# Kernel optimization log

Measured on AMD Instinct MI355X. Metric: run time of the kernel, lower is better.

## Reference

```python
import jax, jax.numpy as jnp
import numpy as np

TOP_K = 48
NUM_RBF = 16
MAX_REL = 32  # max_relative_feature


def _rbf(D):
    # D: [...], expand into NUM_RBF Gaussian basis functions over [2, 22] Angstrom
    mu = jnp.linspace(2.0, 22.0, NUM_RBF)
    sigma = (22.0 - 2.0) / NUM_RBF
    return jnp.exp(-(((D[..., None] - mu) / sigma) ** 2))


def _gather_nodes(C, E_idx):
    # C: [B,L,3], E_idx: [B,L,K] -> [B,L,K,3]
    return jax.vmap(lambda c, idx: c[idx])(C, E_idx)


def _pair_rbf(A, Bc, E_idx):
    # RBF of ||A_i - Bc_j|| for j in neighbors(i); identical math to torch's
    # full [B,L,L] cdist followed by gather_edges, but gathers coords first.
    Bg = _gather_nodes(Bc, E_idx)
    D = jnp.sqrt(jnp.sum((A[:, :, None, :] - Bg) ** 2, -1) + 1e-6)
    return _rbf(D)


def setup_inputs() -> dict:
    key = jax.random.key(0)
    ks = jax.random.split(key, 8)
    B, L = 4, 1024
    X = jax.random.normal(ks[0], (B, L, 4, 3), jnp.float32)
    mask = jnp.ones((B, L), jnp.float32)
    residue_idx = jnp.arange(B * L, dtype=jnp.int32).reshape(B, L)
    chain_labels = jax.random.randint(ks[1], (B, L), 0, 4, dtype=jnp.int32)
    W_pos = jax.random.normal(ks[2], (16, 2 * MAX_REL + 2), jnp.float32) * 0.1
    b_pos = jnp.zeros((16,), jnp.float32)
    W_edge = jax.random.normal(ks[3], (128, 16 + 25 * NUM_RBF), jnp.float32) * 0.05
    ln_g = jnp.ones((128,), jnp.float32)
    ln_b = jnp.zeros((128,), jnp.float32)
    return dict(X=X, mask=mask, residue_idx=residue_idx, chain_labels=chain_labels,
                W_pos=W_pos, b_pos=b_pos, W_edge=W_edge, ln_g=ln_g, ln_b=ln_b)


def reference(X, mask, residue_idx, chain_labels, W_pos, b_pos, W_edge, ln_g, ln_b):
    # backbone atoms
    N = X[:, :, 0]; Ca = X[:, :, 1]; C = X[:, :, 2]; O = X[:, :, 3]
    b = Ca - N
    c = C - Ca
    a = jnp.cross(b, c)
    Cb = -0.58273431 * a + 0.56802827 * b - 0.54067466 * c + Ca

    # _dist: masked Ca-Ca pairwise distances, k nearest neighbors
    mask2 = mask[:, None, :] * mask[:, :, None]          # [B,L,L]
    dX = Ca[:, None, :, :] - Ca[:, :, None, :]
    D = mask2 * jnp.sqrt(jnp.sum(dX ** 2, -1) + 1e-6)
    D_max = jnp.max(D, -1, keepdims=True)
    D_adjust = D + (1.0 - mask2) * D_max
    K = min(TOP_K, X.shape[1])
    negD, E_idx = jax.lax.top_k(-D_adjust, K)            # smallest-K distances
    D_neighbors = -negD                                  # [B,L,K]

    # 25 atom-pair RBF blocks (order matches torch source)
    pairs = [(N, N), (C, C), (O, O), (Cb, Cb), (Ca, N), (Ca, C), (Ca, O), (Ca, Cb),
             (N, C), (N, O), (N, Cb), (Cb, C), (Cb, O), (O, C), (N, Ca), (C, Ca),
             (O, Ca), (Cb, Ca), (C, N), (O, N), (Cb, N), (C, Cb), (O, Cb), (C, O)]
    RBFs = [_rbf(D_neighbors)] + [_pair_rbf(A, Bc, E_idx) for A, Bc in pairs]
    RBFs = jnp.concatenate(RBFs, -1)                     # [B,L,K,25*NUM_RBF]

    # positional encodings
    offset = residue_idx[:, :, None] - residue_idx[:, None, :]
    offset = jnp.take_along_axis(offset, E_idx, axis=2)  # [B,L,K]
    d_chains = (chain_labels[:, :, None] == chain_labels[:, None, :]).astype(jnp.int32)
    E_chains = jnp.take_along_axis(d_chains, E_idx, axis=2)
    d = jnp.clip(offset + MAX_REL, 0, 2 * MAX_REL)
    d = d * E_chains + (1 - E_chains) * (2 * MAX_REL + 1)
    # one_hot(d, 66) @ W_pos.T + b_pos == row gather of W_pos.T
    E_pos = W_pos.T[d] + b_pos                           # [B,L,K,16]

    E = jnp.concatenate([E_pos, RBFs], -1)               # [B,L,K,416]
    E = jnp.einsum('blkf,ef->blke', E, W_edge)           # edge_embedding (no bias)
    mu = jnp.mean(E, -1, keepdims=True)
    var = jnp.var(E, -1, keepdims=True)
    E = (E - mu) / jnp.sqrt(var + 1e-5) * ln_g + ln_b    # LayerNorm
    return E, E_idx
```

## Files before the change

kernel.cpp:

```cpp
#include <hip/hip_runtime.h>
#include <stdint.h>

#define LSEQ 1024
#define NB 4
#define KNB 48
#define NFEAT 416
#define NOUT 128
#define NNODE (NB*LSEQ)

typedef float f32x4 __attribute__((ext_vector_type(4)));
typedef short s16x8 __attribute__((ext_vector_type(8)));

__device__ float4 g_atoms[NNODE*5];
__device__ ushort g_wbf[NOUT*NFEAT];
__device__ ushort g_wpt[66*16];
__device__ int    g_nbr[NNODE*KNB];
__device__ float  g_dnb[NNODE*KNB];

__constant__ int cPA[24] = {0,2,3,4,1,1,1,1,0,0,0,4,4,3,0,2,3,4,2,3,4,2,3,2};
__constant__ int cPB[24] = {0,2,3,4,0,2,3,4,2,3,4,2,3,2,1,1,1,1,0,0,0,4,4,3};

__device__ __forceinline__ ushort f2bf(float x) {
  unsigned u = __float_as_uint(x);
  u += 0x7fffu + ((u >> 16) & 1u);
  return (ushort)(u >> 16);
}
__device__ __forceinline__ unsigned pack2bf(float lo, float hi) {
  return __builtin_amdgcn_perm(__float_as_uint(hi), __float_as_uint(lo), 0x07060302u);
}

#define DPP_ADD_F(x, CTRL) { int _y = __builtin_amdgcn_mov_dpp(__float_as_int(x), CTRL, 0xF, 0xF, true); x += __int_as_float(_y); }
#define DPP_MIN_U(x, CTRL) { unsigned _y = (unsigned)__builtin_amdgcn_mov_dpp((int)(x), CTRL, 0xF, 0xF, true); x = min(x, _y); }

__device__ __forceinline__ unsigned wave_umin(unsigned x) {
  DPP_MIN_U(x, 0x128) DPP_MIN_U(x, 0x124) DPP_MIN_U(x, 0x122) DPP_MIN_U(x, 0x121)
  x = min(x, (unsigned)__shfl_xor((int)x, 16, 64));
  x = min(x, (unsigned)__shfl_xor((int)x, 32, 64));
  return x;
}

__global__ __launch_bounds__(256) void k_front(
    const float* __restrict__ X, const float* __restrict__ mask,
    const float* __restrict__ W, const float* __restrict__ Wpos,
    const float* __restrict__ bpos, float* __restrict__ outIdx)
{
  __shared__ float4 sca[LSEQ];
  __shared__ unsigned qhi[4][64][17];
  __shared__ unsigned qlo[4][64][17];
  int blk = blockIdx.x, tid = threadIdx.x;

  if (blk >= 1024) {
    int pb = blk - 1024;
    if (pb < 16) {
      int t = pb*256 + tid;
      const float* p = X + (size_t)t*12;
      float nx=p[0],ny=p[1],nz=p[2];
      float cax=p[3],cay=p[4],caz=p[5];
      float cx=p[6],cy=p[7],cz=p[8];
      float ox=p[9],oy=p[10],oz=p[11];
      float bx=cax-nx, by=cay-ny, bz=caz-nz;
      float ex=cx-cax, ey=cy-cay, ez=cz-caz;
      float ax2 = by*ez - bz*ey;
      float ay2 = bz*ex - bx*ez;
      float az2 = bx*ey - by*ex;
      float cbx = -0.58273431f*ax2 + 0.56802827f*bx - 0.54067466f*ex + cax;
      float cby = -0.58273431f*ay2 + 0.56802827f*by - 0.54067466f*ey + cay;
      float cbz = -0.58273431f*az2 + 0.56802827f*bz - 0.54067466f*ez + caz;
      g_atoms[t*5+0] = make_float4(nx,ny,nz,0.f);
      g_atoms[t*5+1] = make_float4(cax,cay,caz,0.f);
      g_atoms[t*5+2] = make_float4(cx,cy,cz,0.f);
      g_atoms[t*5+3] = make_float4(ox,oy,oz,0.f);
      g_atoms[t*5+4] = make_float4(cbx,cby,cbz,0.f);
    } else if (pb < 32) {
      int base = (pb-16)*3328 + tid;
      #pragma unroll
      for (int q = 0; q < 13; ++q) g_wbf[base + q*256] = f2bf(W[base + q*256]);
    } else {
      for (int t = tid; t < 66*16; t += 256) {
        int d = t >> 4, c = t & 15;
        g_wpt[t] = f2bf(Wpos[c*66 + d] + bpos[c]);
      }
    }
    return;
  }

  int b = blk >> 8, chunk = blk & 255;
  for (int t = tid; t < LSEQ; t += 256) {
    const float* p = X + (size_t)(b*LSEQ + t)*12 + 3;
    sca[t] = make_float4(p[0], p[1], p[2], mask[b*LSEQ + t]);
  }
  __syncthreads();
  int wv = tid >> 6, lane = tid & 63;
  int i = chunk*4 + wv;
  float4 ci = sca[i];
  float  mi = ci.w;

  float Dv[16]; float dmax = 0.f;
  #pragma unroll
  for (int q = 0; q < 16; ++q) {
    int j = lane + (q << 6);
    float4 cj = sca[j];
    float dx = __fsub_rn(cj.x, ci.x);
    float dy = __fsub_rn(cj.y, ci.y);
    float dz = __fsub_rn(cj.z, ci.z);
    float s  = __fadd_rn(__fadd_rn(__fmul_rn(dx,dx), __fmul_rn(dy,dy)), __fmul_rn(dz,dz));
    float sq = __fsqrt_rn(__fadd_rn(s, 1e-6f));
    float d  = __fmul_rn(__fmul_rn(mi, cj.w), sq);
    Dv[q] = d;
    dmax = fmaxf(dmax, d);
  }
  #pragma unroll
  for (int o = 32; o; o >>= 1) dmax = fmaxf(dmax, __shfl_xor(dmax, o, 64));

  unsigned long long key[16];
  #pragma unroll
  for (int q = 0; q < 16; ++q) {
    int j = lane + (q << 6);
    float m2   = __fmul_rn(mi, sca[j].w);
    float dadj = __fadd_rn(Dv[q], __fmul_rn(__fsub_rn(1.0f, m2), dmax));
    key[q] = ((unsigned long long)__float_as_uint(dadj) << 32) | (unsigned)j;
  }

  #pragma unroll
  for (int p = 1; p < 16; p <<= 1)
    #pragma unroll
    for (int k = p; k >= 1; k >>= 1)
      #pragma unroll
      for (int j = k & (p - 1); j + k < 16; j += 2*k)
        #pragma unroll
        for (int u = 0; u < k; ++u)
          if (u + j + k < 16 && ((u + j) / (2*p) == (u + j + k) / (2*p))) {
            unsigned long long a = key[u+j], c2 = key[u+j+k];
            if (a > c2) { key[u+j] = c2; key[u+j+k] = a; }
          }

  #pragma unroll
  for (int q = 0; q < 16; ++q) {
    qhi[wv][lane][q] = (unsigned)(key[q] >> 32);
    qlo[wv][lane][q] = (unsigned)key[q];
  }

  unsigned hhi = (unsigned)(key[0] >> 32), hlo = (unsigned)key[0];
  int pos = 0;
  size_t row = (size_t)(b*LSEQ + i);
  for (int k = 0; k < KNB; ++k) {
    unsigned mh = wave_umin(hhi);
    unsigned long long bmask = __ballot(hhi == mh);
    bool own;
    if (__popcll(bmask) == 1) {
      own = (hhi == mh);
    } else {
      unsigned jv = (hhi == mh) ? hlo : 0xFFFFFFFFu;
      unsigned mj = wave_umin(jv);
      own = (hhi == mh) && (hlo == mj);
    }
    if (own) {
      g_nbr[row*KNB + k] = (int)hlo;
      g_dnb[row*KNB + k] = __uint_as_float(mh);
      outIdx[row*KNB + k] = (float)(int)hlo;
      ++pos;
      if (pos < 16) { hhi = qhi[wv][lane][pos]; hlo = qlo[wv][lane][pos]; }
      else          { hhi = 0xFFFFFFFFu; hlo = 0xFFFFFFFFu; }
    }
  }
}

__global__ __launch_bounds__(256, 4) void k_edge(
    const int* __restrict__ ridx, const int* __restrict__ chain,
    const float* __restrict__ lng, const float* __restrict__ lnb,
    float* __restrict__ out)
{
  __shared__ __align__(16) ushort featb[KNB*256];
  __shared__ float4 atN[KNB*5];
  __shared__ float4 atI[5];
  __shared__ float  sdn[KNB];
  __shared__ int    sdd[KNB];
  __shared__ float2 sstat[KNB][4];
  __shared__ float2 rstat[KNB];

  int node = blockIdx.x;
  int b = node >> 10;
  size_t ebase = (size_t)node * KNB;
  int t = threadIdx.x;

  if (t < KNB) {
    int j = g_nbr[ebase + t];
    sdn[t] = g_dnb[ebase + t];
    int off = ridx[node] - ridx[b*LSEQ + j];
    bool same = (chain[node] == chain[b*LSEQ + j]);
    int dcl = min(max(off + 32, 0), 64);
    sdd[t] = same ? dcl : 65;
  }
  if (t >= 64 && t < 69) atI[t-64] = g_atoms[node*5 + (t-64)];
  for (int u = t; u < KNB*5; u += 256) {
    int k = u / 5, a = u % 5;
    atN[u] = g_atoms[(b*LSEQ + g_nbr[ebase + k])*5 + a];
  }
  __syncthreads();

  auto rbf_store = [&](int k, int slot, float d) {
    const float DLT  = 1.28119724f;
    const float TDLT = 2.56239448f;
    const float NDSQ = -1.64146638f;
    const float INVK = 0.10274013f;
    float u0  = __fmaf_rn(d, 0.96089793f, -1.92179585f);
    float u15 = u0 - 19.21795854f;
    float e[16];
    float eA = __builtin_amdgcn_exp2f(-(u0*u0));
    float rA = __builtin_amdgcn_exp2f(__fmaf_rn(u0, TDLT, NDSQ));
    float eB = __builtin_amdgcn_exp2f(-(u15*u15));
    float rB = __builtin_amdgcn_exp2f(__fmaf_rn(u15, -TDLT, NDSQ));
    e[0] = eA; e[15] = eB;
    #pragma unroll
    for (int j2 = 1; j2 < 8; ++j2) {
      eA *= rA; rA *= INVK; e[j2] = eA;
      eB *= rB; rB *= INVK; e[15-j2] = eB;
    }
    union { s16x8 v; unsigned w[4]; } a0, a1;
    #pragma unroll
    for (int q = 0; q < 4; ++q) {
      a0.w[q] = pack2bf(e[2*q],   e[2*q+1]);
      a1.w[q] = pack2bf(e[8+2*q], e[8+2*q+1]);
    }
    ushort* fp = &featb[k*256 + ((slot ^ (k & 7)) << 4)];
    *(s16x8*)fp       = a0.v;
    *(s16x8*)(fp + 8) = a1.v;
  };

  if (t < 96) {
    int k = t >> 1, h = t & 1;
    *(s16x8*)&featb[k*256 + ((0 ^ (k & 7)) << 4) + h*8] =
        *(const s16x8*)&g_wpt[sdd[k]*16 + h*8];
  }
  for (int u = t; u < KNB*13; u += 256) {
    int k = u / 13, p = u % 13;
    float d;
    if (p == 0) d = sdn[k];
    else {
      float4 A = atI[cPA[p-1]];
      float4 Bv = atN[k*5 + cPB[p-1]];
      float dx = A.x-Bv.x, dy = A.y-Bv.y, dz = A.z-Bv.z;
      d = sqrtf(dx*dx + dy*dy + dz*dz + 1e-6f);
    }
    rbf_store(k, p + 1, d);
  }
  __syncthreads();

  int ln = t & 63, wv = t >> 6;
  int fr = ln & 15, fq = ln >> 4;
  int n0 = wv * 32;
  f32x4 acc[3][2];
  #pragma unroll
  for (int mt = 0; mt < 3; ++mt) { acc[mt][0] = (f32x4)0.f; acc[mt][1] = (f32x4)0.f; }
  const ushort* w0 = &g_wbf[(n0 + fr)*NFEAT];
  const ushort* w1 = &g_wbf[(n0 + 16 + fr)*NFEAT];

#define GEMM_PASS(WOFF, NSTEPS)                                                     \
  {                                                                                 \
    s16x8 cw0 = *(const s16x8*)&w0[(WOFF) + fq*8];                                  \
    s16x8 cw1 = *(const s16x8*)&w1[(WOFF) + fq*8];                                  \
    _Pragma("unroll")                                                               \
    for (int s = 0; s < (NSTEPS); ++s) {                                            \
      int kk = s*32 + fq*8;                                                         \
      s16x8 nw0, nw1;                                                               \
      if (s + 1 < (NSTEPS)) {                                                       \
        nw0 = *(const s16x8*)&w0[(WOFF) + kk + 32];                                 \
        nw1 = *(const s16x8*)&w1[(WOFF) + kk + 32];                                 \
      }                                                                             \
      _Pragma("unroll")                                                             \
      for (int mt = 0; mt < 3; ++mt) {                                              \
        int row = mt*16 + fr;                                                       \
        s16x8 af = *(const s16x8*)&featb[row*256 + (((kk >> 4) ^ (fr & 7)) << 4) + (kk & 8)]; \
        acc[mt][0] = __builtin_amdgcn_mfma_f32_16x16x32_bf16(af, cw0, acc[mt][0], 0, 0, 0);   \
        acc[mt][1] = __builtin_amdgcn_mfma_f32_16x16x32_bf16(af, cw1, acc[mt][1], 0, 0, 0);   \
      }                                                                             \
      if (s + 1 < (NSTEPS)) { cw0 = nw0; cw1 = nw1; }                               \
    }                                                                               \
  }

  GEMM_PASS(0, 7)
  __syncthreads();

  for (int u = t; u < KNB*12; u += 256) {
    int k = u / 12, p = 13 + u % 12;
    float4 A = atI[cPA[p-1]];
    float4 Bv = atN[k*5 + cPB[p-1]];
    float dx = A.x-Bv.x, dy = A.y-Bv.y, dz = A.z-Bv.z;
    rbf_store(k, p - 13, sqrtf(dx*dx + dy*dy + dz*dz + 1e-6f));
  }
  __syncthreads();

  GEMM_PASS(224, 6)

  #pragma unroll
  for (int mt = 0; mt < 3; ++mt)
    #pragma unroll
    for (int i2 = 0; i2 < 4; ++i2) {
      float v0 = acc[mt][0][i2], v1 = acc[mt][1][i2];
      float s = v0 + v1, sq = v0*v0 + v1*v1;
      DPP_ADD_F(s, 0x128) DPP_ADD_F(s, 0x124) DPP_ADD_F(s, 0x122) DPP_ADD_F(s, 0x121)
      DPP_ADD_F(sq, 0x128) DPP_ADD_F(sq, 0x124) DPP_ADD_F(sq, 0x122) DPP_ADD_F(sq, 0x121)
      if (fr == 0) sstat[mt*16 + fq*4 + i2][wv] = make_float2(s, sq);
    }
  __syncthreads();
  if (t < KNB) {
    float s = 0.f, sq = 0.f;
    #pragma unroll
    for (int w = 0; w < 4; ++w) { float2 pp = sstat[t][w]; s += pp.x; sq += pp.y; }
    float mu  = s * (1.0f/128.0f);
    float var = sq * (1.0f/128.0f) - mu*mu;
    rstat[t] = make_float2(mu, rsqrtf(var + 1e-5f));
  }
  __syncthreads();
  float gn0 = lng[n0+fr], gn1 = lng[n0+16+fr];
  float bn0 = lnb[n0+fr], bn1 = lnb[n0+16+fr];
  #pragma unroll
  for (int mt = 0; mt < 3; ++mt)
    #pragma unroll
    for (int i2 = 0; i2 < 4; ++i2) {
      int row = mt*16 + fq*4 + i2;
      float2 mr = rstat[row];
      size_t ob = (ebase + row) * NOUT;
      out[ob + n0 + fr]      = (acc[mt][0][i2] - mr.x) * mr.y * gn0 + bn0;
      out[ob + n0 + 16 + fr] = (acc[mt][1][i2] - mr.x) * mr.y * gn1 + bn1;
    }
}

extern "C" void kernel_launch(void* const* d_in, const int* in_sizes, int n_in,
                              void* d_out, int out_size, void* d_ws, size_t ws_size,
                              hipStream_t stream) {
  const float* X     = (const float*)d_in[0];
  const float* mask  = (const float*)d_in[1];
  const int*   ridx  = (const int*)d_in[2];
  const int*   chain = (const int*)d_in[3];
  const float* Wpos  = (const float*)d_in[4];
  const float* bpos  = (const float*)d_in[5];
  const float* Wedge = (const float*)d_in[6];
  const float* lng   = (const float*)d_in[7];
  const float* lnb   = (const float*)d_in[8];
  float* out = (float*)d_out;
  float* outIdx = out + (size_t)NNODE*KNB*NOUT;

  k_front<<<dim3(1024 + 33), dim3(256), 0, stream>>>(X, mask, Wedge, Wpos, bpos, outIdx);
  k_edge<<<dim3(NNODE), dim3(256), 0, stream>>>(ridx, chain, lng, lnb, out);
}
```

Before: 81.52 us.

## Split front kernel and replace sorted-queue top-k with per-lane min selection

The fused front kernel is split into separate prep, weight-convert and top-k kernels. The top-k no longer bitonic-sorts each lane's 16 keys into shared-memory queues. Instead each lane keeps only its running minimum, and the wave does a full 64-bit butterfly min reduction each iteration. The owning lane then rescans its 16 registers to find its next minimum. This removes the sort and the LDS queue traffic, but adds two extra kernel launches and a costlier 6-step 64-bit shuffle reduction on each of the 48 iterations.

```diff
diff --git a/kernel.cpp b/kernel.cpp
--- a/kernel.cpp
+++ b/kernel.cpp
@@ -12,6 +12,7 @@
 typedef short s16x8 __attribute__((ext_vector_type(8)));
 
 __device__ float4 g_atoms[NNODE*5];
+__device__ float4 g_ca[NNODE];
 __device__ ushort g_wbf[NOUT*NFEAT];
 __device__ ushort g_wpt[66*16];
 __device__ int    g_nbr[NNODE*KNB];
@@ -30,72 +31,68 @@
 }
 
 #define DPP_ADD_F(x, CTRL) { int _y = __builtin_amdgcn_mov_dpp(__float_as_int(x), CTRL, 0xF, 0xF, true); x += __int_as_float(_y); }
-#define DPP_MIN_U(x, CTRL) { unsigned _y = (unsigned)__builtin_amdgcn_mov_dpp((int)(x), CTRL, 0xF, 0xF, true); x = min(x, _y); }
-
-__device__ __forceinline__ unsigned wave_umin(unsigned x) {
-  DPP_MIN_U(x, 0x128) DPP_MIN_U(x, 0x124) DPP_MIN_U(x, 0x122) DPP_MIN_U(x, 0x121)
-  x = min(x, (unsigned)__shfl_xor((int)x, 16, 64));
-  x = min(x, (unsigned)__shfl_xor((int)x, 32, 64));
-  return x;
-}
-
-__global__ __launch_bounds__(256) void k_front(
-    const float* __restrict__ X, const float* __restrict__ mask,
-    const float* __restrict__ W, const float* __restrict__ Wpos,
-    const float* __restrict__ bpos, float* __restrict__ outIdx)
-{
+
+__device__ __forceinline__ unsigned long long shfl_xor_u64(unsigned long long x, int m) {
+  unsigned hi = __shfl_xor((unsigned)(x >> 32), m, 64);
+  unsigned lo = __shfl_xor((unsigned)(x & 0xffffffffu), m, 64);
+  return ((unsigned long long)hi << 32) | lo;
+}
+
+__global__ void k_prep(const float* __restrict__ X) {
+  int t = blockIdx.x*256 + threadIdx.x;
+  if (t >= NNODE) return;
+  const float* p = X + (size_t)t*12;
+  float nx=p[0],ny=p[1],nz=p[2];
+  float cax=p[3],cay=p[4],caz=p[5];
+  float cx=p[6],cy=p[7],cz=p[8];
+  float ox=p[9],oy=p[10],oz=p[11];
+  float bx=cax-nx, by=cay-ny, bz=caz-nz;
+  float ex=cx-cax, ey=cy-cay, ez=cz-caz;
+  float ax2 = by*ez - bz*ey;
+  float ay2 = bz*ex - bx*ez;
+  float az2 = bx*ey - by*ex;
+  float cbx = -0.58273431f*ax2 + 0.56802827f*bx - 0.54067466f*ex + cax;
+  float cby = -0.58273431f*ay2 + 0.56802827f*by - 0.54067466f*ey + cay;
+  float cbz = -0.58273431f*az2 + 0.56802827f*bz - 0.54067466f*ez + caz;
+  g_atoms[t*5+0] = make_float4(nx,ny,nz,0.f);
+  g_atoms[t*5+1] = make_float4(cax,cay,caz,0.f);
+  g_atoms[t*5+2] = make_float4(cx,cy,cz,0.f);
+  g_atoms[t*5+3] = make_float4(ox,oy,oz,0.f);
+  g_atoms[t*5+4] = make_float4(cbx,cby,cbz,0.f);
+  g_ca[t] = make_float4(cax,cay,caz,0.f);
+}
+
+__global__ void k_wcvt(const float* __restrict__ W, const float* __restrict__ Wpos,
+                       const float* __restrict__ bpos) {
+  int blk = blockIdx.x, tid = threadIdx.x;
+  if (blk < 208) {
+    int t = blk*256 + tid;
+    g_wbf[t] = f2bf(W[t]);
+  } else {
+    for (int t = tid; t < 66*16; t += 256) {
+      int d = t >> 4, c = t & 15;
+      g_wpt[t] = f2bf(Wpos[c*66 + d] + bpos[c]);
+    }
+  }
+}
+
+__global__ __launch_bounds__(256) void k_topk(const float* __restrict__ mask,
+                                              float* __restrict__ outIdx) {
   __shared__ float4 sca[LSEQ];
-  __shared__ unsigned qhi[4][64][17];
-  __shared__ unsigned qlo[4][64][17];
-  int blk = blockIdx.x, tid = threadIdx.x;
-
-  if (blk >= 1024) {
-    int pb = blk - 1024;
-    if (pb < 16) {
-      int t = pb*256 + tid;
-      const float* p = X + (size_t)t*12;
-      float nx=p[0],ny=p[1],nz=p[2];
-      float cax=p[3],cay=p[4],caz=p[5];
-      float cx=p[6],cy=p[7],cz=p[8];
-      float ox=p[9],oy=p[10],oz=p[11];
-      float bx=cax-nx, by=cay-ny, bz=caz-nz;
-      float ex=cx-cax, ey=cy-cay, ez=cz-caz;
-      float ax2 = by*ez - bz*ey;
-      float ay2 = bz*ex - bx*ez;
-      float az2 = bx*ey - by*ex;
-      float cbx = -0.58273431f*ax2 + 0.56802827f*bx - 0.54067466f*ex + cax;
-      float cby = -0.58273431f*ay2 + 0.56802827f*by - 0.54067466f*ey + cay;
-      float cbz = -0.58273431f*az2 + 0.56802827f*bz - 0.54067466f*ez + caz;
-      g_atoms[t*5+0] = make_float4(nx,ny,nz,0.f);
-      g_atoms[t*5+1] = make_float4(cax,cay,caz,0.f);
-      g_atoms[t*5+2] = make_float4(cx,cy,cz,0.f);
-      g_atoms[t*5+3] = make_float4(ox,oy,oz,0.f);
-      g_atoms[t*5+4] = make_float4(cbx,cby,cbz,0.f);
-    } else if (pb < 32) {
-      int base = (pb-16)*3328 + tid;
-      #pragma unroll
-      for (int q = 0; q < 13; ++q) g_wbf[base + q*256] = f2bf(W[base + q*256]);
-    } else {
-      for (int t = tid; t < 66*16; t += 256) {
-        int d = t >> 4, c = t & 15;
-        g_wpt[t] = f2bf(Wpos[c*66 + d] + bpos[c]);
-      }
-    }
-    return;
-  }
-
-  int b = blk >> 8, chunk = blk & 255;
-  for (int t = tid; t < LSEQ; t += 256) {
-    const float* p = X + (size_t)(b*LSEQ + t)*12 + 3;
-    sca[t] = make_float4(p[0], p[1], p[2], mask[b*LSEQ + t]);
-  }
-  __syncthreads();
-  int wv = tid >> 6, lane = tid & 63;
-  int i = chunk*4 + wv;
+  __shared__ float  sm[LSEQ];
+  int b = blockIdx.y;
+  for (int t = threadIdx.x; t < LSEQ; t += 256) {
+    sca[t] = g_ca[b*LSEQ + t];
+    sm[t]  = mask[b*LSEQ + t];
+  }
+  __syncthreads();
+  int wave = threadIdx.x >> 6, lane = threadIdx.x & 63;
+  int i = blockIdx.x*4 + wave;
   float4 ci = sca[i];
-  float  mi = ci.w;
-
-  float Dv[16]; float dmax = 0.f;
+  float  mi = sm[i];
+
+  float Dv[16];
+  float dmax = 0.f;
   #pragma unroll
   for (int q = 0; q < 16; ++q) {
     int j = lane + (q << 6);
@@ -105,7 +102,7 @@
     float dz = __fsub_rn(cj.z, ci.z);
     float s  = __fadd_rn(__fadd_rn(__fmul_rn(dx,dx), __fmul_rn(dy,dy)), __fmul_rn(dz,dz));
     float sq = __fsqrt_rn(__fadd_rn(s, 1e-6f));
-    float d  = __fmul_rn(__fmul_rn(mi, cj.w), sq);
+    float d  = __fmul_rn(__fmul_rn(mi, sm[j]), sq);
     Dv[q] = d;
     dmax = fmaxf(dmax, d);
   }
@@ -113,54 +110,38 @@
   for (int o = 32; o; o >>= 1) dmax = fmaxf(dmax, __shfl_xor(dmax, o, 64));
 
   unsigned long long key[16];
+  unsigned long long lmin = ~0ull;
   #pragma unroll
   for (int q = 0; q < 16; ++q) {
     int j = lane + (q << 6);
-    float m2   = __fmul_rn(mi, sca[j].w);
+    float m2   = __fmul_rn(mi, sm[j]);
     float dadj = __fadd_rn(Dv[q], __fmul_rn(__fsub_rn(1.0f, m2), dmax));
     key[q] = ((unsigned long long)__float_as_uint(dadj) << 32) | (unsigned)j;
-  }
-
-  #pragma unroll
-  for (int p = 1; p < 16; p <<= 1)
-    #pragma unroll
-    for (int k = p; k >= 1; k >>= 1)
-      #pragma unroll
-      for (int j = k & (p - 1); j + k < 16; j += 2*k)
-        #pragma unroll
-        for (int u = 0; u < k; ++u)
-          if (u + j + k < 16 && ((u + j) / (2*p) == (u + j + k) / (2*p))) {
-            unsigned long long a = key[u+j], c2 = key[u+j+k];
-            if (a > c2) { key[u+j] = c2; key[u+j+k] = a; }
-          }
-
-  #pragma unroll
-  for (int q = 0; q < 16; ++q) {
-    qhi[wv][lane][q] = (unsigned)(key[q] >> 32);
-    qlo[wv][lane][q] = (unsigned)key[q];
-  }
-
-  unsigned hhi = (unsigned)(key[0] >> 32), hlo = (unsigned)key[0];
-  int pos = 0;
+    lmin = (key[q] < lmin) ? key[q] : lmin;
+  }
+
   size_t row = (size_t)(b*LSEQ + i);
   for (int k = 0; k < KNB; ++k) {
-    unsigned mh = wave_umin(hhi);
-    unsigned long long bmask = __ballot(hhi == mh);
-    bool own;
-    if (__popcll(bmask) == 1) {
-      own = (hhi == mh);
-    } else {
-      unsigned jv = (hhi == mh) ? hlo : 0xFFFFFFFFu;
-      unsigned mj = wave_umin(jv);
-      own = (hhi == mh) && (hlo == mj);
-    }
-    if (own) {
-      g_nbr[row*KNB + k] = (int)hlo;
-      g_dnb[row*KNB + k] = __uint_as_float(mh);
-      outIdx[row*KNB + k] = (float)(int)hlo;
-      ++pos;
-      if (pos < 16) { hhi = qhi[wv][lane][pos]; hlo = qlo[wv][lane][pos]; }
-      else          { hhi = 0xFFFFFFFFu; hlo = 0xFFFFFFFFu; }
+    unsigned long long m = lmin;
+    #pragma unroll
+    for (int o = 1; o < 64; o <<= 1) {
+      unsigned long long other = shfl_xor_u64(m, o);
+      m = (other < m) ? other : m;
+    }
+    if (lane == 0) {
+      unsigned j = (unsigned)(m & 0xffffffffu);
+      g_nbr[row*KNB + k] = (int)j;
+      g_dnb[row*KNB + k] = __uint_as_float((unsigned)(m >> 32));
+      outIdx[row*KNB + k] = (float)(int)j;
+    }
+    if (m == lmin) {
+      unsigned long long nm = ~0ull;
+      #pragma unroll
+      for (int q = 0; q < 16; ++q) {
+        if (key[q] == m) key[q] = ~0ull;
+        nm = (key[q] < nm) ? key[q] : nm;
+      }
+      lmin = nm;
     }
   }
 }
@@ -199,7 +180,6 @@
   __syncthreads();
 
   auto rbf_store = [&](int k, int slot, float d) {
-    const float DLT  = 1.28119724f;
     const float TDLT = 2.56239448f;
     const float NDSQ = -1.64146638f;
     const float INVK = 0.10274013f;
@@ -341,6 +321,8 @@
   float* out = (float*)d_out;
   float* outIdx = out + (size_t)NNODE*KNB*NOUT;
 
-  k_front<<<dim3(1024 + 33), dim3(256), 0, stream>>>(X, mask, Wedge, Wpos, bpos, outIdx);
+  k_prep<<<dim3(NNODE/256), dim3(256), 0, stream>>>(X);
+  k_wcvt<<<dim3(209), dim3(256), 0, stream>>>(Wedge, Wpos, bpos);
+  k_topk<<<dim3(LSEQ/4, NB), dim3(256), 0, stream>>>(mask, outIdx);
   k_edge<<<dim3(NNODE), dim3(256), 0, stream>>>(ridx, chain, lng, lnb, out);
 }
```

After: 118.2 us. 1.45x slower.

## Fuse kNN top-k selection into edge kernel, drop neighbor index round trip

Applied to the files above, without the earlier changes.

Moves the Ca distance computation, bitonic sort and wave-level top-k merge out of the front kernel and into each edge block, where one wave selects the node's 48 neighbors into shared memory, reusing the feature buffer. A small preprocessing kernel now only builds atoms, Ca coordinates and bf16 weights. This removes the global writes and reads of neighbor indices and distances, along with a large front grid. In exchange, each edge block does its top-k in a single wave while the other three wait, which adds serial latency per block and may lengthen the edge kernel.

```diff
diff --git a/kernel.cpp b/kernel.cpp
--- a/kernel.cpp
+++ b/kernel.cpp
@@ -12,10 +12,9 @@
 typedef short s16x8 __attribute__((ext_vector_type(8)));
 
 __device__ float4 g_atoms[NNODE*5];
+__device__ float4 g_ca[NNODE];
 __device__ ushort g_wbf[NOUT*NFEAT];
 __device__ ushort g_wpt[66*16];
-__device__ int    g_nbr[NNODE*KNB];
-__device__ float  g_dnb[NNODE*KNB];
 
 __constant__ int cPA[24] = {0,2,3,4,1,1,1,1,0,0,0,4,4,3,0,2,3,4,2,3,4,2,3,2};
 __constant__ int cPB[24] = {0,2,3,4,0,2,3,4,2,3,4,2,3,2,1,1,1,1,0,0,0,4,4,3};
@@ -39,167 +38,162 @@
   return x;
 }
 
-__global__ __launch_bounds__(256) void k_front(
-    const float* __restrict__ X, const float* __restrict__ mask,
-    const float* __restrict__ W, const float* __restrict__ Wpos,
-    const float* __restrict__ bpos, float* __restrict__ outIdx)
-{
-  __shared__ float4 sca[LSEQ];
-  __shared__ unsigned qhi[4][64][17];
-  __shared__ unsigned qlo[4][64][17];
+__global__ void k_pre(const float* __restrict__ X, const float* __restrict__ W,
+                      const float* __restrict__ Wpos, const float* __restrict__ bpos) {
   int blk = blockIdx.x, tid = threadIdx.x;
-
-  if (blk >= 1024) {
-    int pb = blk - 1024;
-    if (pb < 16) {
-      int t = pb*256 + tid;
-      const float* p = X + (size_t)t*12;
-      float nx=p[0],ny=p[1],nz=p[2];
-      float cax=p[3],cay=p[4],caz=p[5];
-      float cx=p[6],cy=p[7],cz=p[8];
-      float ox=p[9],oy=p[10],oz=p[11];
-      float bx=cax-nx, by=cay-ny, bz=caz-nz;
-      float ex=cx-cax, ey=cy-cay, ez=cz-caz;
-      float ax2 = by*ez - bz*ey;
-      float ay2 = bz*ex - bx*ez;
-      float az2 = bx*ey - by*ex;
-      float cbx = -0.58273431f*ax2 + 0.56802827f*bx - 0.54067466f*ex + cax;
-      float cby = -0.58273431f*ay2 + 0.56802827f*by - 0.54067466f*ey + cay;
-      float cbz = -0.58273431f*az2 + 0.56802827f*bz - 0.54067466f*ez + caz;
-      g_atoms[t*5+0] = make_float4(nx,ny,nz,0.f);
-      g_atoms[t*5+1] = make_float4(cax,cay,caz,0.f);
-      g_atoms[t*5+2] = make_float4(cx,cy,cz,0.f);
-      g_atoms[t*5+3] = make_float4(ox,oy,oz,0.f);
-      g_atoms[t*5+4] = make_float4(cbx,cby,cbz,0.f);
-    } else if (pb < 32) {
-      int base = (pb-16)*3328 + tid;
-      #pragma unroll
-      for (int q = 0; q < 13; ++q) g_wbf[base + q*256] = f2bf(W[base + q*256]);
-    } else {
-      for (int t = tid; t < 66*16; t += 256) {
-        int d = t >> 4, c = t & 15;
-        g_wpt[t] = f2bf(Wpos[c*66 + d] + bpos[c]);
-      }
-    }
-    return;
-  }
-
-  int b = blk >> 8, chunk = blk & 255;
-  for (int t = tid; t < LSEQ; t += 256) {
-    const float* p = X + (size_t)(b*LSEQ + t)*12 + 3;
-    sca[t] = make_float4(p[0], p[1], p[2], mask[b*LSEQ + t]);
-  }
-  __syncthreads();
-  int wv = tid >> 6, lane = tid & 63;
-  int i = chunk*4 + wv;
-  float4 ci = sca[i];
-  float  mi = ci.w;
-
-  float Dv[16]; float dmax = 0.f;
-  #pragma unroll
-  for (int q = 0; q < 16; ++q) {
-    int j = lane + (q << 6);
-    float4 cj = sca[j];
-    float dx = __fsub_rn(cj.x, ci.x);
-    float dy = __fsub_rn(cj.y, ci.y);
-    float dz = __fsub_rn(cj.z, ci.z);
-    float s  = __fadd_rn(__fadd_rn(__fmul_rn(dx,dx), __fmul_rn(dy,dy)), __fmul_rn(dz,dz));
-    float sq = __fsqrt_rn(__fadd_rn(s, 1e-6f));
-    float d  = __fmul_rn(__fmul_rn(mi, cj.w), sq);
-    Dv[q] = d;
-    dmax = fmaxf(dmax, d);
-  }
-  #pragma unroll
-  for (int o = 32; o; o >>= 1) dmax = fmaxf(dmax, __shfl_xor(dmax, o, 64));
-
-  unsigned long long key[16];
-  #pragma unroll
-  for (int q = 0; q < 16; ++q) {
-    int j = lane + (q << 6);
-    float m2   = __fmul_rn(mi, sca[j].w);
-    float dadj = __fadd_rn(Dv[q], __fmul_rn(__fsub_rn(1.0f, m2), dmax));
-    key[q] = ((unsigned long long)__float_as_uint(dadj) << 32) | (unsigned)j;
-  }
-
-  #pragma unroll
-  for (int p = 1; p < 16; p <<= 1)
-    #pragma unroll
-    for (int k = p; k >= 1; k >>= 1)
-      #pragma unroll
-      for (int j = k & (p - 1); j + k < 16; j += 2*k)
-        #pragma unroll
-        for (int u = 0; u < k; ++u)
-          if (u + j + k < 16 && ((u + j) / (2*p) == (u + j + k) / (2*p))) {
-            unsigned long long a = key[u+j], c2 = key[u+j+k];
-            if (a > c2) { key[u+j] = c2; key[u+j+k] = a; }
-          }
-
-  #pragma unroll
-  for (int q = 0; q < 16; ++q) {
-    qhi[wv][lane][q] = (unsigned)(key[q] >> 32);
-    qlo[wv][lane][q] = (unsigned)key[q];
-  }
-
-  unsigned hhi = (unsigned)(key[0] >> 32), hlo = (unsigned)key[0];
-  int pos = 0;
-  size_t row = (size_t)(b*LSEQ + i);
-  for (int k = 0; k < KNB; ++k) {
-    unsigned mh = wave_umin(hhi);
-    unsigned long long bmask = __ballot(hhi == mh);
-    bool own;
-    if (__popcll(bmask) == 1) {
-      own = (hhi == mh);
-    } else {
-      unsigned jv = (hhi == mh) ? hlo : 0xFFFFFFFFu;
-      unsigned mj = wave_umin(jv);
-      own = (hhi == mh) && (hlo == mj);
-    }
-    if (own) {
-      g_nbr[row*KNB + k] = (int)hlo;
-      g_dnb[row*KNB + k] = __uint_as_float(mh);
-      outIdx[row*KNB + k] = (float)(int)hlo;
-      ++pos;
-      if (pos < 16) { hhi = qhi[wv][lane][pos]; hlo = qlo[wv][lane][pos]; }
-      else          { hhi = 0xFFFFFFFFu; hlo = 0xFFFFFFFFu; }
+  if (blk < 16) {
+    int t = blk*256 + tid;
+    const float* p = X + (size_t)t*12;
+    float nx=p[0],ny=p[1],nz=p[2];
+    float cax=p[3],cay=p[4],caz=p[5];
+    float cx=p[6],cy=p[7],cz=p[8];
+    float ox=p[9],oy=p[10],oz=p[11];
+    float bx=cax-nx, by=cay-ny, bz=caz-nz;
+    float ex=cx-cax, ey=cy-cay, ez=cz-caz;
+    float ax2 = by*ez - bz*ey;
+    float ay2 = bz*ex - bx*ez;
+    float az2 = bx*ey - by*ex;
+    float cbx = -0.58273431f*ax2 + 0.56802827f*bx - 0.54067466f*ex + cax;
+    float cby = -0.58273431f*ay2 + 0.56802827f*by - 0.54067466f*ey + cay;
+    float cbz = -0.58273431f*az2 + 0.56802827f*bz - 0.54067466f*ez + caz;
+    g_atoms[t*5+0] = make_float4(nx,ny,nz,0.f);
+    g_atoms[t*5+1] = make_float4(cax,cay,caz,0.f);
+    g_atoms[t*5+2] = make_float4(cx,cy,cz,0.f);
+    g_atoms[t*5+3] = make_float4(ox,oy,oz,0.f);
+    g_atoms[t*5+4] = make_float4(cbx,cby,cbz,0.f);
+    g_ca[t] = make_float4(cax,cay,caz,0.f);
+  } else if (blk < 224) {
+    int t = (blk-16)*256 + tid;
+    g_wbf[t] = f2bf(W[t]);
+  } else {
+    for (int t = tid; t < 66*16; t += 256) {
+      int d = t >> 4, c = t & 15;
+      g_wpt[t] = f2bf(Wpos[c*66 + d] + bpos[c]);
     }
   }
 }
 
 __global__ __launch_bounds__(256, 4) void k_edge(
+    const float* __restrict__ mask,
     const int* __restrict__ ridx, const int* __restrict__ chain,
     const float* __restrict__ lng, const float* __restrict__ lnb,
-    float* __restrict__ out)
+    float* __restrict__ out, float* __restrict__ outIdx)
 {
-  __shared__ __align__(16) ushort featb[KNB*256];
+  __shared__ __align__(16) unsigned char smem[KNB*256*2];
+  ushort*   featb = (ushort*)smem;
+  float4*   sca   = (float4*)smem;
+  unsigned* qhi   = (unsigned*)(smem + 16384);
+  unsigned* qlo   = (unsigned*)(smem + 16384 + 4096);
   __shared__ float4 atN[KNB*5];
   __shared__ float4 atI[5];
   __shared__ float  sdn[KNB];
+  __shared__ int    snbr[KNB];
   __shared__ int    sdd[KNB];
   __shared__ float2 sstat[KNB][4];
   __shared__ float2 rstat[KNB];
 
   int node = blockIdx.x;
   int b = node >> 10;
+  int irow = node & 1023;
   size_t ebase = (size_t)node * KNB;
   int t = threadIdx.x;
+  int ln = t & 63, wv = t >> 6;
+
+  for (int u = t; u < LSEQ; u += 256) {
+    float4 c = g_ca[b*LSEQ + u];
+    c.w = mask[b*LSEQ + u];
+    sca[u] = c;
+  }
+  if (t >= 64 && t < 69) atI[t-64] = g_atoms[node*5 + (t-64)];
+  __syncthreads();
+
+  if (wv == 0) {
+    float4 ci = sca[irow];
+    float  mi = ci.w;
+    float Dv[16]; float dmax = 0.f;
+    #pragma unroll
+    for (int q = 0; q < 16; ++q) {
+      int j = ln + (q << 6);
+      float4 cj = sca[j];
+      float dx = __fsub_rn(cj.x, ci.x);
+      float dy = __fsub_rn(cj.y, ci.y);
+      float dz = __fsub_rn(cj.z, ci.z);
+      float s  = __fadd_rn(__fadd_rn(__fmul_rn(dx,dx), __fmul_rn(dy,dy)), __fmul_rn(dz,dz));
+      float sq = __fsqrt_rn(__fadd_rn(s, 1e-6f));
+      float d  = __fmul_rn(__fmul_rn(mi, cj.w), sq);
+      Dv[q] = d;
+      dmax = fmaxf(dmax, d);
+    }
+    #pragma unroll
+    for (int o = 32; o; o >>= 1) dmax = fmaxf(dmax, __shfl_xor(dmax, o, 64));
+
+    unsigned long long key[16];
+    #pragma unroll
+    for (int q = 0; q < 16; ++q) {
+      int j = ln + (q << 6);
+      float m2   = __fmul_rn(mi, sca[j].w);
+      float dadj = __fadd_rn(Dv[q], __fmul_rn(__fsub_rn(1.0f, m2), dmax));
+      key[q] = ((unsigned long long)__float_as_uint(dadj) << 32) | (unsigned)j;
+    }
+
+    #pragma unroll
+    for (int p = 1; p < 16; p <<= 1)
+      #pragma unroll
+      for (int k = p; k >= 1; k >>= 1)
+        #pragma unroll
+        for (int j = k & (p - 1); j + k < 16; j += 2*k)
+          #pragma unroll
+          for (int u = 0; u < k; ++u)
+            if (u + j + k < 16 && ((u + j) / (2*p) == (u + j + k) / (2*p))) {
+              unsigned long long a = key[u+j], c2 = key[u+j+k];
+              if (a > c2) { key[u+j] = c2; key[u+j+k] = a; }
+            }
+
+    #pragma unroll
+    for (int q = 0; q < 16; ++q) {
+      qhi[q*64 + ln] = (unsigned)(key[q] >> 32);
+      qlo[q*64 + ln] = (unsigned)key[q];
+    }
+
+    unsigned hhi = (unsigned)(key[0] >> 32), hlo = (unsigned)key[0];
+    int pos = 0;
+    for (int k = 0; k < KNB; ++k) {
+      unsigned mh = wave_umin(hhi);
+      unsigned long long bmask = __ballot(hhi == mh);
+      bool own;
+      if (__popcll(bmask) == 1) {
+        own = (hhi == mh);
+      } else {
+        unsigned jv = (hhi == mh) ? hlo : 0xFFFFFFFFu;
+        unsigned mj = wave_umin(jv);
+        own = (hhi == mh) && (hlo == mj);
+      }
+      if (own) {
+        snbr[k] = (int)hlo;
+        sdn[k]  = __uint_as_float(mh);
+        outIdx[ebase + k] = (float)(int)hlo;
+        ++pos;
+        if (pos < 16) { hhi = qhi[pos*64 + ln]; hlo = qlo[pos*64 + ln]; }
+        else          { hhi = 0xFFFFFFFFu; hlo = 0xFFFFFFFFu; }
+      }
+    }
+  }
+  __syncthreads();
 
   if (t < KNB) {
-    int j = g_nbr[ebase + t];
-    sdn[t] = g_dnb[ebase + t];
+    int j = snbr[t];
     int off = ridx[node] - ridx[b*LSEQ + j];
     bool same = (chain[node] == chain[b*LSEQ + j]);
     int dcl = min(max(off + 32, 0), 64);
     sdd[t] = same ? dcl : 65;
   }
-  if (t >= 64 && t < 69) atI[t-64] = g_atoms[node*5 + (t-64)];
   for (int u = t; u < KNB*5; u += 256) {
     int k = u / 5, a = u % 5;
-    atN[u] = g_atoms[(b*LSEQ + g_nbr[ebase + k])*5 + a];
+    atN[u] = g_atoms[(b*LSEQ + snbr[k])*5 + a];
   }
   __syncthreads();
 
   auto rbf_store = [&](int k, int slot, float d) {
-    const float DLT  = 1.28119724f;
     const float TDLT = 2.56239448f;
     const float NDSQ = -1.64146638f;
     const float INVK = 0.10274013f;
@@ -246,7 +240,6 @@
   }
   __syncthreads();
 
-  int ln = t & 63, wv = t >> 6;
   int fr = ln & 15, fq = ln >> 4;
   int n0 = wv * 32;
   f32x4 acc[3][2];
@@ -341,6 +334,6 @@
   float* out = (float*)d_out;
   float* outIdx = out + (size_t)NNODE*KNB*NOUT;
 
-  k_front<<<dim3(1024 + 33), dim3(256), 0, stream>>>(X, mask, Wedge, Wpos, bpos, outIdx);
-  k_edge<<<dim3(NNODE), dim3(256), 0, stream>>>(ridx, chain, lng, lnb, out);
-}
+  k_pre<<<dim3(225), dim3(256), 0, stream>>>(X, Wedge, Wpos, bpos);
+  k_edge<<<dim3(NNODE), dim3(256), 0, stream>>>(mask, ridx, chain, lng, lnb, out, outIdx);
+}
```

After: 102.9 us. 26.3% more time.
